# Optimization experiments

Measured on AMD Instinct MI355X. Metric: run time of the kernel, lower is better.

## Reference

```python
import jax, jax.numpy as jnp
import numpy as np

VOCAB = 100000
DIM = 128
B = 16384
K = 20


def setup_inputs() -> dict:
    key = jax.random.key(0)
    k1, k2, k3, k4, k5 = jax.random.split(key, 5)
    initrange = np.sqrt(2.0 / (VOCAB + DIM)).astype(np.float32)
    return {
        "center_words": jax.random.randint(k1, (B, 1), 0, VOCAB),
        "target_words": jax.random.randint(k2, (B, 1), 0, VOCAB),
        "negative_words": jax.random.randint(k3, (B, K), 0, VOCAB),
        "V": jax.random.uniform(k4, (VOCAB, DIM), jnp.float32, -initrange, initrange),
        "U": jax.random.uniform(k5, (VOCAB, DIM), jnp.float32, -initrange, initrange),
    }


def reference(center_words, target_words, negative_words, V, U):
    # gathers: center from V table, target/negative from U table
    ce = V[center_words[:, 0]]        # [B, D]
    te = U[target_words[:, 0]]        # [B, D]
    ne = U[negative_words]            # [B, K, D]

    pos_score = jnp.sum(te * ce, axis=-1)                # [B]  (bmm [B,1,D]x[B,D,1])
    neg_scores = jnp.einsum("bkd,bd->bk", ne, ce)        # [B, K]

    pos_ls = jax.nn.log_sigmoid(pos_score)               # [B]
    neg_ls_sum = jnp.sum(jax.nn.log_sigmoid(-neg_scores), axis=1)  # [B]

    # Original torch code broadcasts [B,1] + [B] -> [B,B] then means; since
    # mean(a_i + b_j) == mean(a) + mean(b), compute the identical value
    # without materializing the BxB intermediate.
    loss = -(jnp.mean(pos_ls) + jnp.mean(neg_ls_sum))
    return loss
```

## Files before the change

kernel.cpp:

```cpp
#include <hip/hip_runtime.h>

#define B_SIZE 16384
#define K_NEG 20
#define DIM 128
#define NROWS (K_NEG + 1)
#define CHUNK 7

__device__ __forceinline__ float logsig(float x) {
    return fminf(x, 0.0f) - __logf(1.0f + __expf(-fabsf(x)));
}

__device__ __forceinline__ float dot8(float4 a0, float4 a1, float4 b0, float4 b1) {
    return a0.x * b0.x + a0.y * b0.y + a0.z * b0.z + a0.w * b0.w
         + a1.x * b1.x + a1.y * b1.y + a1.z * b1.z + a1.w * b1.w;
}

__global__ __launch_bounds__(256, 4) void skipgram_loss_kernel(
    const int* __restrict__ center,
    const int* __restrict__ target,
    const int* __restrict__ neg,
    const float* __restrict__ V,
    const float* __restrict__ U,
    float* __restrict__ accum)
{
    const int tid  = threadIdx.x;
    const int lane = tid & 63;
    const int wid  = tid >> 6;
    const int sub  = lane >> 4;
    const int sl   = lane & 15;

    const int e = blockIdx.x * 16 + wid * 4 + sub;

    int idx[NROWS];
    idx[0] = target[e];
    {
        const int* nb = neg + e * K_NEG;
        #pragma unroll
        for (int k = 0; k < K_NEG; ++k) idx[k + 1] = nb[k];
    }

    const int c = center[e];
    const float4* vrow = (const float4*)(V + (size_t)c * DIM);
    const float4 c0 = vrow[sl * 2];
    const float4 c1 = vrow[sl * 2 + 1];

    float acc = 0.0f;
    #pragma unroll
    for (int ch = 0; ch < 3; ++ch) {
        float4 a0[CHUNK], a1[CHUNK];
        #pragma unroll
        for (int r = 0; r < CHUNK; ++r) {
            const float4* ur = (const float4*)(U + (size_t)idx[ch * CHUNK + r] * DIM) + sl * 2;
            a0[r] = ur[0];
            a1[r] = ur[1];
        }
        __builtin_amdgcn_sched_barrier(0);

        float part[CHUNK];
        #pragma unroll
        for (int r = 0; r < CHUNK; ++r)
            part[r] = dot8(c0, c1, a0[r], a1[r]);

        #pragma unroll
        for (int s = 1; s < 16; s <<= 1) {
            #pragma unroll
            for (int r = 0; r < CHUNK; ++r)
                part[r] += __shfl_xor(part[r], s, 64);
        }

        #pragma unroll
        for (int r = 0; r < CHUNK; ++r) {
            const bool positive = (ch == 0 && r == 0);
            acc += logsig(positive ? part[r] : -part[r]);
        }
    }

    float v = (sl == 0) ? acc : 0.0f;
    v += __shfl_xor(v, 16, 64);
    v += __shfl_xor(v, 32, 64);

    __shared__ float ssum[4];
    if (lane == 0) ssum[wid] = v;
    __syncthreads();
    if (tid == 0)
        atomicAdd(accum, ssum[0] + ssum[1] + ssum[2] + ssum[3]);
}

__global__ void finalize_kernel(const float* __restrict__ accum,
                                float* __restrict__ out)
{
    out[0] = -accum[0] * (1.0f / (float)B_SIZE);
}

extern "C" void kernel_launch(void* const* d_in, const int* in_sizes, int n_in,
                              void* d_out, int out_size, void* d_ws, size_t ws_size,
                              hipStream_t stream) {
    const int*   center = (const int*)d_in[0];
    const int*   target = (const int*)d_in[1];
    const int*   neg    = (const int*)d_in[2];
    const float* V      = (const float*)d_in[3];
    const float* U      = (const float*)d_in[4];
    float* out   = (float*)d_out;
    float* accum = (float*)d_ws;

    hipMemsetAsync(accum, 0, sizeof(float), stream);

    skipgram_loss_kernel<<<B_SIZE / 16, 256, 0, stream>>>(center, target, neg, V, U, accum);
    finalize_kernel<<<1, 1, 0, stream>>>(accum, out);
}
```

Before: 40.51 us.

## Use 32 lanes per example with float4 rows and prefetched neg indices

Each example is now handled by 32 lanes, each loading one float4 per row, instead of 16 lanes loading two, which doubles the grid and lowers register use so the launch bound can ask for 8 waves. The negative indices for the next chunk are loaded while the current chunk's rows are in flight, rather than all 21 indices being held up front. The aim is more memory-level parallelism and occupancy for this gather-bound kernel. In exchange each reduction needs one more shuffle stage, and twice as many blocks each do an atomic add.

Result: slower. 50.29 us (+24.1%).

```diff
diff --git a/kernel.cpp b/kernel.cpp
--- a/kernel.cpp
+++ b/kernel.cpp
@@ -3,19 +3,14 @@
 #define B_SIZE 16384
 #define K_NEG 20
 #define DIM 128
-#define NROWS (K_NEG + 1)
+#define NROWS 21
 #define CHUNK 7
 
 __device__ __forceinline__ float logsig(float x) {
     return fminf(x, 0.0f) - __logf(1.0f + __expf(-fabsf(x)));
 }
 
-__device__ __forceinline__ float dot8(float4 a0, float4 a1, float4 b0, float4 b1) {
-    return a0.x * b0.x + a0.y * b0.y + a0.z * b0.z + a0.w * b0.w
-         + a1.x * b1.x + a1.y * b1.y + a1.z * b1.z + a1.w * b1.w;
-}
-
-__global__ __launch_bounds__(256, 4) void skipgram_loss_kernel(
+__global__ __launch_bounds__(256, 8) void skipgram_loss_kernel(
     const int* __restrict__ center,
     const int* __restrict__ target,
     const int* __restrict__ neg,
@@ -26,57 +21,59 @@
     const int tid  = threadIdx.x;
     const int lane = tid & 63;
     const int wid  = tid >> 6;
-    const int sub  = lane >> 4;
-    const int sl   = lane & 15;
+    const int sub  = lane >> 5;
+    const int sl   = lane & 31;
 
-    const int e = blockIdx.x * 16 + wid * 4 + sub;
+    const int e = blockIdx.x * 8 + wid * 2 + sub;
 
-    int idx[NROWS];
-    idx[0] = target[e];
-    {
-        const int* nb = neg + e * K_NEG;
-        #pragma unroll
-        for (int k = 0; k < K_NEG; ++k) idx[k + 1] = nb[k];
-    }
+    const float4 ce = ((const float4*)(V + (size_t)center[e] * DIM))[sl];
 
-    const int c = center[e];
-    const float4* vrow = (const float4*)(V + (size_t)c * DIM);
-    const float4 c0 = vrow[sl * 2];
-    const float4 c1 = vrow[sl * 2 + 1];
+    const int* nb = neg + e * K_NEG;
+
+    int idxc[CHUNK];
+    idxc[0] = target[e];
+    #pragma unroll
+    for (int r = 1; r < CHUNK; ++r) idxc[r] = nb[r - 1];
 
     float acc = 0.0f;
     #pragma unroll
     for (int ch = 0; ch < 3; ++ch) {
-        float4 a0[CHUNK], a1[CHUNK];
+        float4 a[CHUNK];
         #pragma unroll
-        for (int r = 0; r < CHUNK; ++r) {
-            const float4* ur = (const float4*)(U + (size_t)idx[ch * CHUNK + r] * DIM) + sl * 2;
-            a0[r] = ur[0];
-            a1[r] = ur[1];
+        for (int r = 0; r < CHUNK; ++r)
+            a[r] = ((const float4*)(U + (size_t)idxc[r] * DIM))[sl];
+
+        int idxn[CHUNK];
+        if (ch < 2) {
+            #pragma unroll
+            for (int r = 0; r < CHUNK; ++r)
+                idxn[r] = nb[(ch + 1) * CHUNK + r - 1];
         }
         __builtin_amdgcn_sched_barrier(0);
 
         float part[CHUNK];
         #pragma unroll
         for (int r = 0; r < CHUNK; ++r)
-            part[r] = dot8(c0, c1, a0[r], a1[r]);
+            part[r] = a[r].x * ce.x + a[r].y * ce.y + a[r].z * ce.z + a[r].w * ce.w;
 
         #pragma unroll
-        for (int s = 1; s < 16; s <<= 1) {
+        for (int s = 1; s < 32; s <<= 1) {
             #pragma unroll
             for (int r = 0; r < CHUNK; ++r)
                 part[r] += __shfl_xor(part[r], s, 64);
         }
 
         #pragma unroll
-        for (int r = 0; r < CHUNK; ++r) {
-            const bool positive = (ch == 0 && r == 0);
-            acc += logsig(positive ? part[r] : -part[r]);
+        for (int r = 0; r < CHUNK; ++r)
+            acc += logsig((ch == 0 && r == 0) ? part[r] : -part[r]);
+
+        if (ch < 2) {
+            #pragma unroll
+            for (int r = 0; r < CHUNK; ++r) idxc[r] = idxn[r];
         }
     }
 
     float v = (sl == 0) ? acc : 0.0f;
-    v += __shfl_xor(v, 16, 64);
     v += __shfl_xor(v, 32, 64);
 
     __shared__ float ssum[4];
@@ -105,6 +102,6 @@
 
     hipMemsetAsync(accum, 0, sizeof(float), stream);
 
-    skipgram_loss_kernel<<<B_SIZE / 16, 256, 0, stream>>>(center, target, neg, V, U, accum);
+    skipgram_loss_kernel<<<B_SIZE / 8, 256, 0, stream>>>(center, target, neg, V, U, accum);
     finalize_kernel<<<1, 1, 0, stream>>>(accum, out);
 }
```
